# Kernel optimization log

Hardware: AMD Instinct MI355X
Metric: run time of the kernel (lower is better)

The kernel has to match this reference:

```python
import jax, jax.numpy as jnp
import numpy as np

N_CLASSES = 16384
M = 2
D = 128


def setup_inputs() -> dict:
    key = jax.random.key(0)
    k1, k2 = jax.random.split(key)
    x = jax.random.normal(k1, (N_CLASSES * M, D), dtype=jnp.float32)
    anchor_idx = jax.random.randint(k2, (N_CLASSES,), 0, M, dtype=jnp.int64 if jax.config.jax_enable_x64 else jnp.int32).astype(jnp.int32)
    pos_idx = (1 - anchor_idx).astype(jnp.int32)  # randperm(2) -> positive is the other sample
    return {"x": x, "anchor_idx": anchor_idx, "pos_idx": pos_idx}


def reference(x, anchor_idx, pos_idx):
    # x: [N*M, D]; anchor_idx/pos_idx: [N] in [0, M)
    N = anchor_idx.shape[0]
    Dx = x.shape[1]
    xr = x.reshape(N, M, Dx)
    anchors = jnp.take_along_axis(xr, anchor_idx[:, None, None], axis=1)[:, 0, :]    # [N, D]
    positives = jnp.take_along_axis(xr, pos_idx[:, None, None], axis=1)[:, 0, :]     # [N, D]
    negs = xr[:, 1, :]                                                               # [N, D] (sample 1 of every class)
    # score[i, j] = a_i . (neg_j - pos_i) = a_i . neg_j - a_i . pos_i
    S = anchors @ negs.T                                                             # [N, N]
    ap = jnp.sum(anchors * positives, axis=1)                                        # [N]
    logits = S - ap[:, None]
    mask = ~jnp.eye(N, dtype=bool)                                                   # exclude j == i (own class)
    sums = jnp.sum(jnp.where(mask, jnp.exp(logits), jnp.float32(0.0)), axis=1)       # [N]
    return jnp.sum(jnp.log1p(sums))
```

## Files before the change

### kernel.cpp

```cpp
#include <hip/hip_runtime.h>
#include <hip/hip_bf16.h>
#include <math.h>

#define N_CLS 16384
#define DDIM  128
#define LOG2E 1.4426950408889634f

#if __has_builtin(__builtin_amdgcn_exp2f)
#define EXP2(x) __builtin_amdgcn_exp2f(x)
#else
#define EXP2(x) exp2f(x)
#endif

typedef __attribute__((ext_vector_type(8))) short short8;
typedef __attribute__((ext_vector_type(16))) float f32x16;

__device__ __forceinline__ unsigned short f2bf(float f) {
    __hip_bfloat16 h = __float2bfloat16(f);
    return *(unsigned short*)&h;
}

__global__ __launch_bounds__(256)
void prep_kernel(const float* __restrict__ x,
                 const int* __restrict__ aidx,
                 float* __restrict__ ap,
                 unsigned short* __restrict__ Afrag,
                 unsigned short* __restrict__ Bfrag,
                 float* __restrict__ out) {
    const int t = threadIdx.x;
    const int g = blockIdx.x;
    const int lane = t & 63;
    const int w = t >> 6;
    const int m = lane & 31;
    const int half = lane >> 5;
    const int i = g * 32 + m;
    const bool sel = (aidx[i] != 0);

    float d = 0.0f;
    #pragma unroll
    for (int h = 0; h < 2; ++h) {
        const int kc = w * 2 + h;
        const int k0 = kc * 16 + half * 8;
        float fa[8], fb[8];
        *(float4*)&fa[0] = *(const float4*)(x + (2L * i) * DDIM + k0);
        *(float4*)&fa[4] = *(const float4*)(x + (2L * i) * DDIM + k0 + 4);
        *(float4*)&fb[0] = *(const float4*)(x + (2L * i + 1) * DDIM + k0);
        *(float4*)&fb[4] = *(const float4*)(x + (2L * i + 1) * DDIM + k0 + 4);
        short8 As8, Bs8;
        #pragma unroll
        for (int j = 0; j < 8; ++j) {
            const float av = sel ? fb[j] : fa[j];
            As8[j] = (short)f2bf(av * LOG2E);
            Bs8[j] = (short)f2bf(fb[j]);
            d += fa[j] * fb[j];
        }
        *(short8*)(Afrag + (long)g * 4096 + kc * 512 + lane * 8) = As8;
        *(short8*)(Bfrag + (long)g * 4096 + kc * 512 + lane * 8) = Bs8;
    }
    d += __shfl_xor(d, 32, 64);
    __shared__ float sap[4][32];
    if (lane < 32) sap[w][lane] = d;
    __syncthreads();
    if (t < 32) ap[g * 32 + t] = sap[0][t] + sap[1][t] + sap[2][t] + sap[3][t];
    if (t == 0 && g == 0) out[0] = 0.0f;
}

__global__ __launch_bounds__(256, 4)
void fused_kernel(const unsigned short* __restrict__ Afrag,
                  const unsigned short* __restrict__ Bfrag,
                  float* __restrict__ partial) {
    const int tid = threadIdx.x;
    const int lane = tid & 63;
    const int w = tid >> 6;
    const int l31 = lane & 31;
    const int hi = lane >> 5;
    const int oct = blockIdx.x & 7;
    const int rt = blockIdx.x >> 3;
    const int gRow = rt * 4 + w;

    short8 af[8];
    {
        const unsigned short* abase = Afrag + (long)gRow * 4096 + lane * 8;
        #pragma unroll
        for (int kc = 0; kc < 8; ++kc)
            af[kc] = *(const short8*)(abase + kc * 512);
    }
    const unsigned short* bbase = Bfrag + (long)oct * 64 * 4096 + lane * 8;

    const int ctd0 = gRow - oct * 64;
    const int ctd = (ctd0 >= 0 && ctd0 < 64) ? ctd0 : -1;

    float rs[16];
    #pragma unroll
    for (int r = 0; r < 16; ++r) rs[r] = 0.0f;

    short8 bP[4], bQ[4];
    #pragma unroll
    for (int kc = 0; kc < 4; ++kc) bP[kc] = *(const short8*)(bbase + kc * 512);
    #pragma unroll
    for (int kc = 0; kc < 4; ++kc) bQ[kc] = *(const short8*)(bbase + 2048 + kc * 512);

    for (int ct = 0; ct < 64; ++ct) {
        const unsigned short* nb = bbase + (long)((ct < 63) ? ct + 1 : ct) * 4096;

        f32x16 acc;
        #pragma unroll
        for (int r = 0; r < 16; ++r) acc[r] = 0.0f;

        #pragma unroll
        for (int kc = 0; kc < 4; ++kc)
            acc = __builtin_amdgcn_mfma_f32_32x32x16_bf16(af[kc], bP[kc], acc, 0, 0, 0);
        #pragma unroll
        for (int kc = 0; kc < 4; ++kc)
            bP[kc] = *(const short8*)(nb + kc * 512);
        #pragma unroll
        for (int kc = 0; kc < 4; ++kc)
            acc = __builtin_amdgcn_mfma_f32_32x32x16_bf16(af[4 + kc], bQ[kc], acc, 0, 0, 0);
        #pragma unroll
        for (int kc = 0; kc < 4; ++kc)
            bQ[kc] = *(const short8*)(nb + 2048 + kc * 512);

        if (ct == ctd) {
            #pragma unroll
            for (int r = 0; r < 16; ++r) {
                const float e = EXP2(acc[r]);
                const int row = (r & 3) + 8 * (r >> 2) + 4 * hi;
                rs[r] += (l31 == row) ? 0.0f : e;
            }
        } else {
            #pragma unroll
            for (int r = 0; r < 16; ++r) rs[r] += EXP2(acc[r]);
        }
    }

    #pragma unroll
    for (int r = 0; r < 16; ++r) {
        float v = rs[r];
        v += __shfl_xor(v, 1, 64);
        v += __shfl_xor(v, 2, 64);
        v += __shfl_xor(v, 4, 64);
        v += __shfl_xor(v, 8, 64);
        v += __shfl_xor(v, 16, 64);
        if (l31 == 0) {
            const int row = (r & 3) + 8 * (r >> 2) + 4 * hi;
            partial[(long)oct * N_CLS + (long)gRow * 32 + row] = v;
        }
    }
}

__global__ __launch_bounds__(256)
void finalize_kernel(const float* __restrict__ partial,
                     const float* __restrict__ ap,
                     float* __restrict__ out) {
    __shared__ float red[256];
    const int t = threadIdx.x;
    const int row = blockIdx.x * 256 + t;
    float s = 0.0f;
    #pragma unroll
    for (int p = 0; p < 8; ++p) s += partial[(long)p * N_CLS + row];
    const float u = logf(s) - ap[row];
    const float loss = (u > 25.0f) ? u : log1pf(__expf(u));
    red[t] = loss;
    __syncthreads();
    for (int st = 128; st > 0; st >>= 1) {
        if (t < st) red[t] += red[t + st];
        __syncthreads();
    }
    if (t == 0) atomicAdd(out, red[0]);
}

extern "C" void kernel_launch(void* const* d_in, const int* in_sizes, int n_in,
                              void* d_out, int out_size, void* d_ws, size_t ws_size,
                              hipStream_t stream) {
    const float* x    = (const float*)d_in[0];
    const int*   aidx = (const int*)d_in[1];

    char* ws = (char*)d_ws;
    float* ap             = (float*)(ws);
    float* partial        = (float*)(ws + 131072);
    unsigned short* Afrag = (unsigned short*)(ws + 131072 + 1048576);
    unsigned short* Bfrag = (unsigned short*)(ws + 131072 + 1048576 + 4194304);

    prep_kernel<<<N_CLS / 32, 256, 0, stream>>>(x, aidx, ap, Afrag, Bfrag, (float*)d_out);
    fused_kernel<<<1024, 256, 0, stream>>>(Afrag, Bfrag, partial);
    finalize_kernel<<<64, 256, 0, stream>>>(partial, ap, (float*)d_out);
}
```

Measured before the change: 154.9 us.

## Share B tiles through LDS double buffer and compute two row tiles per wave

The fused kernel now stages each 32-column B tile into a double-buffered shared-memory array that all four waves read. Each wave now computes two 32-row tiles against every B fragment, so per-wave global B loads are shared across waves and reused across two MFMA chains, and the grid halves to 512 blocks. The prep kernel is also rewritten so that consecutive threads read contiguous rows of x, which coalesces the loads. In exchange, each tile step adds a block-wide barrier, the extra accumulators raise register pressure (launch bounds drop to 3 blocks per SM), and fewer blocks means less parallelism.

```diff
diff --git a/kernel.cpp b/kernel.cpp
--- a/kernel.cpp
+++ b/kernel.cpp
@@ -29,121 +29,148 @@
                  float* __restrict__ out) {
     const int t = threadIdx.x;
     const int g = blockIdx.x;
-    const int lane = t & 63;
-    const int w = t >> 6;
-    const int m = lane & 31;
-    const int half = lane >> 5;
-    const int i = g * 32 + m;
-    const bool sel = (aidx[i] != 0);
-
-    float d = 0.0f;
-    #pragma unroll
-    for (int h = 0; h < 2; ++h) {
-        const int kc = w * 2 + h;
-        const int k0 = kc * 16 + half * 8;
-        float fa[8], fb[8];
-        *(float4*)&fa[0] = *(const float4*)(x + (2L * i) * DDIM + k0);
-        *(float4*)&fa[4] = *(const float4*)(x + (2L * i) * DDIM + k0 + 4);
-        *(float4*)&fb[0] = *(const float4*)(x + (2L * i + 1) * DDIM + k0);
-        *(float4*)&fb[4] = *(const float4*)(x + (2L * i + 1) * DDIM + k0 + 4);
-        short8 As8, Bs8;
-        #pragma unroll
-        for (int j = 0; j < 8; ++j) {
-            const float av = sel ? fb[j] : fa[j];
-            As8[j] = (short)f2bf(av * LOG2E);
-            Bs8[j] = (short)f2bf(fb[j]);
-            d += fa[j] * fb[j];
-        }
-        *(short8*)(Afrag + (long)g * 4096 + kc * 512 + lane * 8) = As8;
-        *(short8*)(Bfrag + (long)g * 4096 + kc * 512 + lane * 8) = Bs8;
-    }
-    d += __shfl_xor(d, 32, 64);
-    __shared__ float sap[4][32];
-    if (lane < 32) sap[w][lane] = d;
-    __syncthreads();
-    if (t < 32) ap[g * 32 + t] = sap[0][t] + sap[1][t] + sap[2][t] + sap[3][t];
+    #pragma unroll
+    for (int u = 0; u < 4; ++u) {
+        const int l  = u * 256 + t;
+        const int r  = l >> 4;
+        const int k0 = (l & 15) * 8;
+        const float* src = x + (long)g * 8192 + (long)r * 128 + k0;
+        float fa[8];
+        *(float4*)&fa[0] = *(const float4*)(src);
+        *(float4*)&fa[4] = *(const float4*)(src + 4);
+        const long dst = (long)g * 4096 +
+                         ((l & 15) >> 1) * 512 + ((l & 1) * 32 + (r >> 1)) * 8;
+        if (r & 1) {
+            short8 B;
+            #pragma unroll
+            for (int j = 0; j < 8; ++j) B[j] = (short)f2bf(fa[j]);
+            *(short8*)(Bfrag + dst) = B;
+        } else {
+            float fb[8];
+            *(float4*)&fb[0] = *(const float4*)(src + 128);
+            *(float4*)&fb[4] = *(const float4*)(src + 132);
+            const int i = g * 32 + (r >> 1);
+            const bool sel = (aidx[i] != 0);
+            short8 A;
+            float d = 0.0f;
+            #pragma unroll
+            for (int j = 0; j < 8; ++j) {
+                const float av = sel ? fb[j] : fa[j];
+                A[j] = (short)f2bf(av * LOG2E);
+                d += fa[j] * fb[j];
+            }
+            *(short8*)(Afrag + dst) = A;
+            d += __shfl_xor(d, 1, 64);
+            d += __shfl_xor(d, 2, 64);
+            d += __shfl_xor(d, 4, 64);
+            d += __shfl_xor(d, 8, 64);
+            if ((t & 15) == 0) ap[i] = d;
+        }
+    }
     if (t == 0 && g == 0) out[0] = 0.0f;
 }
 
-__global__ __launch_bounds__(256, 4)
+__global__ __launch_bounds__(256, 3)
 void fused_kernel(const unsigned short* __restrict__ Afrag,
                   const unsigned short* __restrict__ Bfrag,
                   float* __restrict__ partial) {
-    const int tid = threadIdx.x;
+    __shared__ __align__(16) unsigned short bs[2][4096];
+    const int tid  = threadIdx.x;
     const int lane = tid & 63;
-    const int w = tid >> 6;
-    const int l31 = lane & 31;
-    const int hi = lane >> 5;
-    const int oct = blockIdx.x & 7;
-    const int rt = blockIdx.x >> 3;
-    const int gRow = rt * 4 + w;
-
-    short8 af[8];
+    const int w    = tid >> 6;
+    const int l31  = lane & 31;
+    const int hi   = lane >> 5;
+    const int oct  = blockIdx.x & 7;
+    const int rt   = blockIdx.x >> 3;
+    const int r0   = rt * 8 + w * 2;
+    const int r1   = r0 + 1;
+
+    short8 af0[8], af1[8];
     {
-        const unsigned short* abase = Afrag + (long)gRow * 4096 + lane * 8;
+        const unsigned short* a0 = Afrag + (long)r0 * 4096 + lane * 8;
+        const unsigned short* a1 = Afrag + (long)r1 * 4096 + lane * 8;
         #pragma unroll
-        for (int kc = 0; kc < 8; ++kc)
-            af[kc] = *(const short8*)(abase + kc * 512);
-    }
-    const unsigned short* bbase = Bfrag + (long)oct * 64 * 4096 + lane * 8;
-
-    const int ctd0 = gRow - oct * 64;
-    const int ctd = (ctd0 >= 0 && ctd0 < 64) ? ctd0 : -1;
-
-    float rs[16];
-    #pragma unroll
-    for (int r = 0; r < 16; ++r) rs[r] = 0.0f;
-
-    short8 bP[4], bQ[4];
-    #pragma unroll
-    for (int kc = 0; kc < 4; ++kc) bP[kc] = *(const short8*)(bbase + kc * 512);
-    #pragma unroll
-    for (int kc = 0; kc < 4; ++kc) bQ[kc] = *(const short8*)(bbase + 2048 + kc * 512);
+        for (int kc = 0; kc < 8; ++kc) {
+            af0[kc] = *(const short8*)(a0 + kc * 512);
+            af1[kc] = *(const short8*)(a1 + kc * 512);
+        }
+    }
+    const unsigned short* bbase = Bfrag + (long)oct * (64L * 4096) + lane * 8;
+    const int wchunk = w * 1024;
+
+    const int ctd0 = r0 - oct * 64;
+    const int ctd1 = r1 - oct * 64;
+
+    float rs0[16], rs1[16];
+    #pragma unroll
+    for (int q = 0; q < 16; ++q) { rs0[q] = 0.0f; rs1[q] = 0.0f; }
+
+    {
+        short8 s0 = *(const short8*)(bbase + wchunk);
+        short8 s1 = *(const short8*)(bbase + wchunk + 512);
+        *(short8*)(&bs[0][wchunk + lane * 8]) = s0;
+        *(short8*)(&bs[0][wchunk + 512 + lane * 8]) = s1;
+    }
+    __syncthreads();
 
     for (int ct = 0; ct < 64; ++ct) {
-        const unsigned short* nb = bbase + (long)((ct < 63) ? ct + 1 : ct) * 4096;
-
-        f32x16 acc;
+        const int cur = ct & 1;
+        const long nt = (ct < 63) ? (long)(ct + 1) : 63L;
+        short8 n0 = *(const short8*)(bbase + nt * 4096 + wchunk);
+        short8 n1 = *(const short8*)(bbase + nt * 4096 + wchunk + 512);
+
+        f32x16 acc0, acc1;
         #pragma unroll
-        for (int r = 0; r < 16; ++r) acc[r] = 0.0f;
-
+        for (int q = 0; q < 16; ++q) { acc0[q] = 0.0f; acc1[q] = 0.0f; }
+
+        const unsigned short* bp = &bs[cur][lane * 8];
         #pragma unroll
-        for (int kc = 0; kc < 4; ++kc)
-            acc = __builtin_amdgcn_mfma_f32_32x32x16_bf16(af[kc], bP[kc], acc, 0, 0, 0);
-        #pragma unroll
-        for (int kc = 0; kc < 4; ++kc)
-            bP[kc] = *(const short8*)(nb + kc * 512);
-        #pragma unroll
-        for (int kc = 0; kc < 4; ++kc)
-            acc = __builtin_amdgcn_mfma_f32_32x32x16_bf16(af[4 + kc], bQ[kc], acc, 0, 0, 0);
-        #pragma unroll
-        for (int kc = 0; kc < 4; ++kc)
-            bQ[kc] = *(const short8*)(nb + 2048 + kc * 512);
-
-        if (ct == ctd) {
-            #pragma unroll
-            for (int r = 0; r < 16; ++r) {
-                const float e = EXP2(acc[r]);
-                const int row = (r & 3) + 8 * (r >> 2) + 4 * hi;
-                rs[r] += (l31 == row) ? 0.0f : e;
+        for (int kc = 0; kc < 8; ++kc) {
+            short8 b = *(const short8*)(bp + kc * 512);
+            acc0 = __builtin_amdgcn_mfma_f32_32x32x16_bf16(af0[kc], b, acc0, 0, 0, 0);
+            acc1 = __builtin_amdgcn_mfma_f32_32x32x16_bf16(af1[kc], b, acc1, 0, 0, 0);
+        }
+
+        if (ct == ctd0) {
+            #pragma unroll
+            for (int q = 0; q < 16; ++q) {
+                const float e = EXP2(acc0[q]);
+                const int row = (q & 3) + 8 * (q >> 2) + 4 * hi;
+                rs0[q] += (l31 == row) ? 0.0f : e;
             }
         } else {
             #pragma unroll
-            for (int r = 0; r < 16; ++r) rs[r] += EXP2(acc[r]);
-        }
-    }
-
-    #pragma unroll
-    for (int r = 0; r < 16; ++r) {
-        float v = rs[r];
-        v += __shfl_xor(v, 1, 64);
-        v += __shfl_xor(v, 2, 64);
-        v += __shfl_xor(v, 4, 64);
-        v += __shfl_xor(v, 8, 64);
-        v += __shfl_xor(v, 16, 64);
+            for (int q = 0; q < 16; ++q) rs0[q] += EXP2(acc0[q]);
+        }
+        if (ct == ctd1) {
+            #pragma unroll
+            for (int q = 0; q < 16; ++q) {
+                const float e = EXP2(acc1[q]);
+                const int row = (q & 3) + 8 * (q >> 2) + 4 * hi;
+                rs1[q] += (l31 == row) ? 0.0f : e;
+            }
+        } else {
+            #pragma unroll
+            for (int q = 0; q < 16; ++q) rs1[q] += EXP2(acc1[q]);
+        }
+
+        *(short8*)(&bs[cur ^ 1][wchunk + lane * 8]) = n0;
+        *(short8*)(&bs[cur ^ 1][wchunk + 512 + lane * 8]) = n1;
+        __syncthreads();
+    }
+
+    #pragma unroll
+    for (int q = 0; q < 16; ++q) {
+        float v0 = rs0[q], v1 = rs1[q];
+        v0 += __shfl_xor(v0, 1, 64);  v1 += __shfl_xor(v1, 1, 64);
+        v0 += __shfl_xor(v0, 2, 64);  v1 += __shfl_xor(v1, 2, 64);
+        v0 += __shfl_xor(v0, 4, 64);  v1 += __shfl_xor(v1, 4, 64);
+        v0 += __shfl_xor(v0, 8, 64);  v1 += __shfl_xor(v1, 8, 64);
+        v0 += __shfl_xor(v0, 16, 64); v1 += __shfl_xor(v1, 16, 64);
         if (l31 == 0) {
-            const int row = (r & 3) + 8 * (r >> 2) + 4 * hi;
-            partial[(long)oct * N_CLS + (long)gRow * 32 + row] = v;
+            const int row = (q & 3) + 8 * (q >> 2) + 4 * hi;
+            partial[(long)oct * N_CLS + (long)r0 * 32 + row] = v0;
+            partial[(long)oct * N_CLS + (long)r1 * 32 + row] = v1;
         }
     }
 }
@@ -182,6 +209,6 @@
     unsigned short* Bfrag = (unsigned short*)(ws + 131072 + 1048576 + 4194304);
 
     prep_kernel<<<N_CLS / 32, 256, 0, stream>>>(x, aidx, ap, Afrag, Bfrag, (float*)d_out);
-    fused_kernel<<<1024, 256, 0, stream>>>(Afrag, Bfrag, partial);
+    fused_kernel<<<512, 256, 0, stream>>>(Afrag, Bfrag, partial);
     finalize_kernel<<<64, 256, 0, stream>>>(partial, ap, (float*)d_out);
 }
```

Result: faster. 141.1 us (-8.9%).
